# Performance work log

Hardware: AMD Instinct MI355X
Metric: run time of the kernel (lower is better)

## Reference

```python
import jax, jax.numpy as jnp
import numpy as np

B, N, K = 2, 8192, 16
D_IN, D_OUT = 32, 128
EPS = 1e-5


def _bn(x, gamma, beta):
    # x: (B, C, L); BatchNorm1d training-mode stats over (B, L)
    mean = x.mean(axis=(0, 2), keepdims=True)
    var = x.var(axis=(0, 2), keepdims=True)
    return gamma[None, :, None] * (x - mean) * jax.lax.rsqrt(var + EPS) + beta[None, :, None]


def _shared_mlp(x, w, b, gamma, beta, act):
    # SharedMLP: 1x1 Conv1d (channel GEMM) + BN + activation. x: (B, Cin, L)
    y = jnp.einsum('oi,bil->bol', w, x) + b[None, :, None]
    return act(_bn(y, gamma, beta))


def _attentive_pool(x, w, b):
    # x: (B, C, N, K); per-(b,n,k) Linear over C, softmax over K, weighted sum over K
    scores = jnp.einsum('oc,bcnk->bonk', w, x) + b[None, :, None, None]
    scores = jax.nn.softmax(scores, axis=-1)
    return jnp.sum(scores * x, axis=-1)  # (B, C, N)  (torch keeps K=1 dim; squeezed by SharedMLP reshape)


def _knn(coords, k):
    # brute-force squared-L2 KNN excluding self (faiss IndexFlatL2 semantics)
    sq = jnp.sum(coords * coords, axis=-1)  # (B, N)
    d2 = sq[:, :, None] + sq[:, None, :] - 2.0 * jnp.einsum('bid,bjd->bij', coords, coords)
    n = coords.shape[1]
    d2 = jnp.where(jnp.eye(n, dtype=bool)[None], jnp.inf, d2)
    neg, idx = jax.lax.top_k(-d2, k)  # ascending squared distance
    return idx, jnp.maximum(-neg, 0.0)


def _lse(coords, features, idx, dist, w, b, gamma, beta):
    # LocalSpatialEncoding: gather neighbor coords, build 10-ch relative features, MLP, concat
    Bq, Nq, Kq = idx.shape
    neighbor = jax.vmap(lambda c, i: c[i])(coords, idx)  # (B, N, K, 3)
    center = jnp.broadcast_to(coords[:, :, None, :], neighbor.shape)
    rel = center - neighbor
    spatial = jnp.concatenate([center, neighbor, rel, dist[..., None]], axis=-1)  # (B, N, K, 10)
    spatial = spatial.transpose(0, 3, 1, 2).reshape(Bq, 10, Nq * Kq)
    sf = _shared_mlp(spatial, w, b, gamma, beta, jax.nn.relu).reshape(Bq, -1, Nq, Kq)
    feat = jnp.broadcast_to(features[..., None], (Bq, features.shape[1], Nq, Kq))
    return jnp.concatenate([sf, feat], axis=1)


def _forward(coords, features,
             mlp1_w, mlp1_b, mlp1_g, mlp1_bt,
             lse1_w, lse1_b, lse1_g, lse1_bt,
             mlpp1_w, mlpp1_b, mlpp1_g, mlpp1_bt,
             lse2_w, lse2_b, lse2_g, lse2_bt,
             mlp2_w, mlp2_b, mlp2_g, mlp2_bt,
             res_w, res_b, res_g, res_bt,
             pool1_w, pool1_b, pool2_w, pool2_b):
    # faiss output is detached in torch (numpy round-trip) -> stop_gradient
    idx, dist = _knn(jax.lax.stop_gradient(coords), K)
    lrelu02 = lambda v: jnp.where(v >= 0, v, 0.2 * v)   # LeakyReLU(0.2)
    lrelu01 = lambda v: jnp.where(v >= 0, v, 0.01 * v)  # default LeakyReLU
    x = _shared_mlp(features, mlp1_w, mlp1_b, mlp1_g, mlp1_bt, lrelu02)      # (B, 64, N)
    x = _lse(coords, x, idx, dist, lse1_w, lse1_b, lse1_g, lse1_bt)          # (B, 128, N, K)
    x = _attentive_pool(x, pool1_w, pool1_b)                                  # (B, 128, N)
    x = _shared_mlp(x, mlpp1_w, mlpp1_b, mlpp1_g, mlpp1_bt, jax.nn.relu)     # (B, 32, N)
    x = _lse(coords, x, idx, dist, lse2_w, lse2_b, lse2_g, lse2_bt)          # (B, 64, N, K)
    x = _attentive_pool(x, pool2_w, pool2_b)                                  # (B, 64, N)
    x_main = _shared_mlp(x, mlp2_w, mlp2_b, mlp2_g, mlp2_bt, jax.nn.relu)    # (B, 128, N)
    resid = _shared_mlp(features, res_w, res_b, res_g, res_bt, jax.nn.relu)  # (B, 128, N)
    return lrelu01(jnp.concatenate([x_main, resid], axis=1))                 # (B, 256, N)


def setup_inputs() -> dict:
    key = jax.random.key(0)
    ks = iter(jax.random.split(key, 64))

    def lin(ci, co):
        w = jax.random.normal(next(ks), (co, ci), jnp.float32) / np.float32(np.sqrt(ci))
        b = jax.random.normal(next(ks), (co,), jnp.float32) * 0.01
        return w, b

    inp = {}
    inp['coords'] = jax.random.normal(next(ks), (B, N, 3), jnp.float32)
    inp['features'] = jax.random.normal(next(ks), (B, D_IN, N), jnp.float32)
    for name, ci, co in [('mlp1', D_IN, D_OUT // 2), ('lse1', 10, D_OUT // 2),
                         ('mlpp1', D_OUT, D_OUT // 4), ('lse2', 10, D_OUT // 4),
                         ('mlp2', D_OUT // 2, D_OUT), ('res', D_IN, D_OUT)]:
        w, b = lin(ci, co)
        inp[name + '_w'], inp[name + '_b'] = w, b
        inp[name + '_g'] = jnp.ones((co,), jnp.float32)
        inp[name + '_bt'] = jnp.zeros((co,), jnp.float32)
    for name, c in [('pool1', D_OUT), ('pool2', D_OUT // 2)]:
        w, b = lin(c, c)
        inp[name + '_w'], inp[name + '_b'] = w, b
    return inp


def reference(coords, features,
              mlp1_w, mlp1_b, mlp1_g, mlp1_bt,
              lse1_w, lse1_b, lse1_g, lse1_bt,
              mlpp1_w, mlpp1_b, mlpp1_g, mlpp1_bt,
              lse2_w, lse2_b, lse2_g, lse2_bt,
              mlp2_w, mlp2_b, mlp2_g, mlp2_bt,
              res_w, res_b, res_g, res_bt,
              pool1_w, pool1_b, pool2_w, pool2_b):
    return _forward(coords, features,
                    mlp1_w, mlp1_b, mlp1_g, mlp1_bt,
                    lse1_w, lse1_b, lse1_g, lse1_bt,
                    mlpp1_w, mlpp1_b, mlpp1_g, mlpp1_bt,
                    lse2_w, lse2_b, lse2_g, lse2_bt,
                    mlp2_w, mlp2_b, mlp2_g, mlp2_bt,
                    res_w, res_b, res_g, res_bt,
                    pool1_w, pool1_b, pool2_w, pool2_b)
```

## Files before the change

kernel.cpp:

```cpp
#include <hip/hip_runtime.h>

static constexpr int N_ = 8192;
static constexpr int B_ = 2;
static constexpr int K_ = 16;

typedef __attribute__((ext_vector_type(8))) short bf16x8;
typedef __attribute__((ext_vector_type(4))) float f32x4;

__device__ __forceinline__ short f2bf(float f) {
  unsigned int u = __float_as_uint(f);
  unsigned int r = (u + 0x7FFFu + ((u >> 16) & 1u)) >> 16;
  return (short)r;
}
__device__ __forceinline__ float bf2f(short h) {
  return __uint_as_float(((unsigned int)(unsigned short)h) << 16);
}

__global__ __launch_bounds__(512) void knn_kernel(const float* __restrict__ coords,
                                                  const int tbeg, const int tend,
                                                  float* __restrict__ skd, int* __restrict__ ski,
                                                  int* __restrict__ oidx, float* __restrict__ odist) {
  __shared__ float4 pts[2048];
  const int b = blockIdx.y;
  const int wv = threadIdx.x >> 6;
  const int lane = threadIdx.x & 63;
  const int q = blockIdx.x * 8 + wv;
  const float* cb = coords + (size_t)b * N_ * 3;
  const float qx = cb[q * 3 + 0], qy = cb[q * 3 + 1], qz = cb[q * 3 + 2];
  const float qsq = fmaf(qx, qx, fmaf(qy, qy, qz * qz));
  const int qblk = q & ~63;
  const unsigned long long qbit = ~(1ull << (q & 63));
  float kd = INFINITY;
  int ki = 0;
  if (tbeg > 0 && lane < 16) {
    kd = skd[((size_t)b * N_ + q) * K_ + lane];
    ki = ski[((size_t)b * N_ + q) * K_ + lane];
  }
  float tau = __shfl(kd, 15);
  for (int t0 = tbeg; t0 < tend; t0 += 2048) {
    __syncthreads();
    for (int i = threadIdx.x; i < 2048; i += 512) {
      const int p = t0 + i;
      const float x = cb[p * 3 + 0], y = cb[p * 3 + 1], z = cb[p * 3 + 2];
      pts[i] = make_float4(x, y, z, fmaf(x, x, fmaf(y, y, z * z)));
    }
    __syncthreads();
    for (int s = 0; s < 2048; s += 64) {
      const float4 p = pts[s + lane];
      const int base = t0 + s;
      const float dot = fmaf(qx, p.x, fmaf(qy, p.y, qz * p.z));
      const float d2 = fmaf(-2.0f, dot, qsq + p.w);
      unsigned long long m = __ballot(d2 < tau);
      if (base == qblk) m &= qbit;
      while (m) {
// ... 1 lines not shown
        const float dc = __shfl(d2, src);
        const int jc = base + src;
        const float sd = __shfl_up(kd, 1);
        const int si = __shfl_up(ki, 1);
        const bool c1 = kd > dc;
        const bool c2 = (lane > 0) && (sd > dc);
        kd = c1 ? (c2 ? sd : dc) : kd;
        ki = c1 ? (c2 ? si : jc) : ki;
        m &= (m - 1);
        tau = __shfl(kd, 15);
        m &= __ballot(d2 < tau);
      }
    }
  }
  if (lane < 16) {
    if (tend < N_) {
      skd[((size_t)b * N_ + q) * K_ + lane] = kd;
      ski[((size_t)b * N_ + q) * K_ + lane] = ki;
    } else {
      oidx[((size_t)b * N_ + q) * K_ + lane] = ki;
      odist[((size_t)b * N_ + q) * K_ + lane] = fmaxf(kd, 0.0f);
    }
  }
}

__device__ __forceinline__ float snn_get(const float* SNN, int a, int b) {
  const int i = a < b ? a : b, j = a < b ? b : a;
  return SNN[i == 0 ? j : (i == 1 ? 2 + j : 3 + j)];
}
__device__ __forceinline__ float mom_mean(int i, const float* C, const float* SN, float Sd) {
  if (i < 3) return 16.0f * C[i];
  if (i < 6) return SN[i - 3];
  if (i < 9) return 16.0f * C[i - 6] - SN[i - 6];
  return Sd;
}
__device__ __forceinline__ float mom_prod(int i, int j, const float* C, const float* SN,
                                          const float* SNN, float Sd, float Sdd, const float* SND) {
// ... 1 lines not shown
  const int tj = j < 3 ? 0 : (j < 6 ? 1 : (j < 9 ? 2 : 3));
  const int a = (ti == 3) ? 0 : (i - ti * 3);
  const int bb = (tj == 3) ? 0 : (j - tj * 3);
  if (ti == 0 && tj == 0) return 16.0f * C[a] * C[bb];
  if (ti == 0 && tj == 1) return C[a] * SN[bb];
  if (ti == 0 && tj == 2) return C[a] * (16.0f * C[bb] - SN[bb]);
  if (ti == 0 && tj == 3) return C[a] * Sd;
  if (ti == 1 && tj == 1) return snn_get(SNN, a, bb);
  if (ti == 1 && tj == 2) return C[bb] * SN[a] - snn_get(SNN, a, bb);
  if (ti == 1 && tj == 3) return SND[a];
  if (ti == 2 && tj == 2) return 16.0f * C[a] * C[bb] - C[a] * SN[bb] - C[bb] * SN[a] + snn_get(SNN, a, bb);
  if (ti == 2 && tj == 3) return C[a] * Sd - SND[a];
  return Sdd;
}

__global__ __launch_bounds__(256) void moments_kernel(const float* __restrict__ coords,
                                                      const int* __restrict__ knn_i,
                                                      const float* __restrict__ knn_d,
                                                      double* __restrict__ mom) {
  __shared__ float sh[16][65];
  const int k = threadIdx.x & 15;
  const int pl = threadIdx.x >> 4;
  float accv = 0.0f;
  for (int batch = 0; batch < 4; ++batch) {
    const int pt = (blockIdx.x * 4 + batch) * 16 + pl;
    const int b = pt >> 13, n = pt & (N_ - 1);
    const float* cb = coords + (size_t)b * N_ * 3;
    const float cx = cb[n * 3 + 0], cy = cb[n * 3 + 1], cz = cb[n * 3 + 2];
    const int id = knn_i[(size_t)pt * K_ + k];
    const float dd = knn_d[(size_t)pt * K_ + k];
    const float nx = cb[id * 3 + 0], ny = cb[id * 3 + 1], nz = cb[id * 3 + 2];
    float v[14] = {nx, ny, nz, nx * nx, nx * ny, nx * nz, ny * ny, ny * nz, nz * nz,
                   dd, dd * dd, nx * dd, ny * dd, nz * dd};
#pragma unroll
    for (int e = 0; e < 14; ++e) {
      v[e] += __shfl_xor(v[e], 1);
      v[e] += __shfl_xor(v[e], 2);
      v[e] += __shfl_xor(v[e], 4);
      v[e] += __shfl_xor(v[e], 8);
    }
    if (k == 0) {
      const float C[3] = {cx, cy, cz};
      const float SN[3] = {v[0], v[1], v[2]};
      const float SNN[6] = {v[3], v[4], v[5], v[6], v[7], v[8]};
      const float Sd = v[9], Sdd = v[10];
      const float SND[3] = {v[11], v[12], v[13]};
      float m65[65];
      int e = 0;
#pragma unroll
      for (int i = 0; i < 10; ++i) m65[e++] = mom_mean(i, C, SN, Sd);
#pragma unroll
      for (int i = 0; i < 10; ++i)
#pragma unroll
        for (int j = i; j < 10; ++j) m65[e++] = mom_prod(i, j, C, SN, SNN, Sd, Sdd, SND);
#pragma unroll
      for (int q2 = 0; q2 < 65; ++q2) sh[pl][q2] = m65[q2];
    }
    __syncthreads();
    if (threadIdx.x < 65) {
      float s = 0.0f;
#pragma unroll
      for (int r = 0; r < 16; ++r) s += sh[r][threadIdx.x];
      accv += s;
    }
    __syncthreads();
  }
  if (threadIdx.x < 65) atomicAdd(&mom[threadIdx.x], (double)accv);
}

template <int CI, int CO>
__device__ __forceinline__ void conv_frag_seg(const float* __restrict__ w, short* __restrict__ H,
                                              short* __restrict__ L, int tid, int nthr) {
  constexpr int NT = CO / 16;
  for (int i = tid; i < CI * CO; i += nthr) {
    const int j = i & 7, l = (i >> 3) & 63, tmp = i >> 9;
    const int tt = tmp % NT, cc = tmp / NT;
    const int c = cc * 32 + (l >> 4) * 8 + j;
    const int o = tt * 16 + (l & 15);
    const float v = w[o * CI + c];
    const short h = f2bf(v);
    H[i] = h;
    L[i] = f2bf(v - bf2f(h));
  }
}

__global__ __launch_bounds__(256) void convert_kernel(
    const float* __restrict__ pw1, const float* __restrict__ pw2,
    short* __restrict__ wB1, short* __restrict__ wB2,
    const float* __restrict__ wm1, short* __restrict__ f1H, short* __restrict__ f1L,
    const float* __restrict__ wmp, short* __restrict__ f2H, short* __restrict__ f2L,
    const float* __restrict__ wm2, short* __restrict__ f3H, short* __restrict__ f3L,
    const float* __restrict__ wrs, short* __restrict__ fRH, short* __restrict__ fRL) {
  const int blk = blockIdx.x;
  if (blk < 8) {
    const int tid = blk * 256 + threadIdx.x;
    for (int i = tid; i < 128 * 128; i += 2048) wB1[i] = f2bf(pw1[i]);
  } else if (blk < 10) {
    const int tid = (blk - 8) * 256 + threadIdx.x;
    for (int i = tid; i < 64 * 64; i += 512) wB2[i] = f2bf(pw2[i]);
  } else if (blk < 12) {
    conv_frag_seg<32, 64>(wm1, f1H, f1L, (blk - 10) * 256 + threadIdx.x, 512);
  } else if (blk < 16) {
    conv_frag_seg<128, 32>(wmp, f2H, f2L, (blk - 12) * 256 + threadIdx.x, 1024);
  } else if (blk < 24) {
    conv_frag_seg<64, 128>(wm2, f3H, f3L, (blk - 16) * 256 + threadIdx.x, 2048);
  } else {
    conv_frag_seg<32, 128>(wrs, fRH, fRL, (blk - 24) * 256 + threadIdx.x, 1024);
  }
}

__global__ void setup_kernel(const double* __restrict__ mom,
                             const float* __restrict__ w1, const float* __restrict__ b1,
                             const float* __restrict__ g1, const float* __restrict__ t1,
                             const float* __restrict__ w2, const float* __restrict__ b2,
                             const float* __restrict__ g2, const float* __restrict__ t2,
                             float* __restrict__ w1f8, float* __restrict__ w2f8) {
  const int t = threadIdx.x;
  __shared__ double mu[10];
  __shared__ double S[10][10];
  const double cnt = (double)B_ * N_ * K_;
  if (t < 10) mu[t] = mom[t] / cnt;
  if (t < 55) {
    int e = t, i = 0;
    while (e >= 10 - i) { e -= 10 - i; ++i; }
    const int j = i + e;
    const double v = mom[10 + t] / cnt;
    S[i][j] = v;
    S[j][i] = v;
  }
  __syncthreads();
  const float *w, *bias, *gg, *bt;
  float *wf;
  int c;
  if (t < 64) { w = w1; bias = b1; gg = g1; bt = t1; wf = w1f8; c = t; }
  else if (t < 96) { w = w2; bias = b2; gg = g2; bt = t2; wf = w2f8; c = t - 64; }
  else return;
  double wd[10];
#pragma unroll
  for (int d = 0; d < 10; ++d) wd[d] = (double)w[c * 10 + d];
  const double cbv = (double)bias[c];
  double mz = cbv;
  for (int d = 0; d < 10; ++d) mz += wd[d] * mu[d];
  double e2 = cbv * cbv;
  for (int d = 0; d < 10; ++d) e2 += 2.0 * cbv * wd[d] * mu[d];
  for (int d = 0; d < 10; ++d)
    for (int e = 0; e < 10; ++e) e2 += wd[d] * wd[e] * S[d][e];
  const double var = e2 - mz * mz;
  const double a = (double)gg[c] / sqrt(var + 1e-5);
  const double shift = (double)bt[c] - a * mz;
  wf[c * 8 + 0] = (float)(a * (wd[0] + wd[6]));
  wf[c * 8 + 1] = (float)(a * (wd[1] + wd[7]));
  wf[c * 8 + 2] = (float)(a * (wd[2] + wd[8]));
  wf[c * 8 + 3] = (float)(a * (wd[3] - wd[6]));
  wf[c * 8 + 4] = (float)(a * (wd[4] - wd[7]));
  wf[c * 8 + 5] = (float)(a * (wd[5] - wd[8]));
  wf[c * 8 + 6] = (float)(a * wd[9]);
  wf[c * 8 + 7] = (float)(a * cbv + shift);
}

template <int CI, int CO, bool ROWMAJ>
__global__ __launch_bounds__(256) void gemm_mfma_kernel(const float* __restrict__ in,
                                                        const short* __restrict__ fragH,
                                                        const short* __restrict__ fragL,
                                                        const float* __restrict__ bias,
                                                        float* __restrict__ out,
                                                        double* __restrict__ sacc) {
  constexpr int NT = CO / 16;
  constexpr int NC = CI / 32;
  __shared__ float part[4][CO][2];
  const int wv = threadIdx.x >> 6, l = threadIdx.x & 63;
  const int col = l & 15, quad = l >> 4;
  const int p0 = blockIdx.x * 64 + wv * 16;
  const int pt = p0 + col;
  f32x4 d[NT];
#pragma unroll
  for (int t = 0; t < NT; ++t) {
    const float bv = bias[t * 16 + col];
    d[t][0] = bv; d[t][1] = bv; d[t][2] = bv; d[t][3] = bv;
  }
#pragma unroll
  for (int cc = 0; cc < NC; ++cc) {
    float xv[8];
    if (ROWMAJ) {
      const float* ip = in + (size_t)pt * CI + cc * 32 + quad * 8;
      *(float4*)&xv[0] = *(const float4*)ip;
      *(float4*)&xv[4] = *(const float4*)(ip + 4);
    } else {
      const int b = pt >> 13, n = pt & (N_ - 1);
      const float* ip = in + ((size_t)b * CI + cc * 32 + quad * 8) * N_ + n;
#pragma unroll
      for (int j = 0; j < 8; ++j) xv[j] = ip[(size_t)j * N_];
    }
    union { bf16x8 v; short u[8]; } AH, AL;
#pragma unroll
    for (int j = 0; j < 8; ++j) {
      const short h = f2bf(xv[j]);
      AH.u[j] = h;
      AL.u[j] = f2bf(xv[j] - bf2f(h));
    }
#pragma unroll
    for (int t = 0; t < NT; ++t) {
      const size_t fo = ((size_t)(cc * NT + t) * 64 + l) * 8;
      const bf16x8 BH = *(const bf16x8*)(fragH + fo);
      const bf16x8 BL = *(const bf16x8*)(fragL + fo);
      d[t] = __builtin_amdgcn_mfma_f32_16x16x32_bf16(AH.v, BH, d[t], 0, 0, 0);
      d[t] = __builtin_amdgcn_mfma_f32_16x16x32_bf16(AH.v, BL, d[t], 0, 0, 0);
      d[t] = __builtin_amdgcn_mfma_f32_16x16x32_bf16(AL.v, BH, d[t], 0, 0, 0);
    }
  }
#pragma unroll
  for (int t = 0; t < NT; ++t) {
#pragma unroll
    for (int r = 0; r < 4; ++r)
      out[(size_t)(p0 + quad * 4 + r) * CO + t * 16 + col] = d[t][r];
    float s1 = d[t][0] + d[t][1] + d[t][2] + d[t][3];
    float s2 = d[t][0] * d[t][0] + d[t][1] * d[t][1] + d[t][2] * d[t][2] + d[t][3] * d[t][3];
    s1 += __shfl_xor(s1, 16); s1 += __shfl_xor(s1, 32);
    s2 += __shfl_xor(s2, 16); s2 += __shfl_xor(s2, 32);
    if (quad == 0) { part[wv][t * 16 + col][0] = s1; part[wv][t * 16 + col][1] = s2; }
  }
  __syncthreads();
  if (threadIdx.x < CO) {
    const int o = threadIdx.x;
    atomicAdd(&sacc[o], (double)(part[0][o][0] + part[1][o][0] + part[2][o][0] + part[3][o][0]));
    atomicAdd(&sacc[CO + o], (double)(part[0][o][1] + part[1][o][1] + part[2][o][1] + part[3][o][1]));
  }
}

template <int CSF, int CF>
__global__ __launch_bounds__(256) void pool_kernel(
    const float* __restrict__ coords, const int* __restrict__ knn_i, const float* __restrict__ knn_d,
    const float* __restrict__ w8,
    const float* __restrict__ feat, const double* __restrict__ sfe,
    const float* __restrict__ gfe, const float* __restrict__ tfe,
    const float slope,
    const short* __restrict__ wB, const float* __restrict__ pb,
    float* __restrict__ out) {
  constexpr int C = CSF + CF;
  constexpr int CP = C + 4;
  constexpr int NT = C / 16;
  constexpr int NC = C / 32;
  __shared__ float xcat[4][16][CP];
  __shared__ float4 sp4[4][16];
  __shared__ float4 spc[4];
  const int g = threadIdx.x >> 6;
  const int l = threadIdx.x & 63;
  const int quad = l >> 4, col = l & 15;
  const int pid = blockIdx.x * 4 + g;
  const int b = pid >> 13, n = pid & (N_ - 1);
  const float* cb = coords + (size_t)b * N_ * 3;

  if (l < 16) {
    const int id = knn_i[(size_t)pid * K_ + l];
    const float dd = knn_d[(size_t)pid * K_ + l];
    const float nx = cb[id * 3 + 0], ny = cb[id * 3 + 1], nz = cb[id * 3 + 2];
    sp4[g][l] = make_float4(nx, ny, nz, dd);
    if (l == 0) spc[g] = make_float4(cb[n * 3 + 0], cb[n * 3 + 1], cb[n * 3 + 2], 0.0f);
  }
  if (l < CF) {
    const double cnt = (double)(B_ * N_);
    const double mean = sfe[l] / cnt;
    const double var = sfe[CF + l] / cnt - mean * mean;
    const double av = (double)gfe[l] / sqrt(var + 1e-5);
    const float af = (float)av;
    const float bfv = (float)((double)tfe[l] - av * mean);
    float v = feat[(size_t)pid * CF + l];
    v = af * v + bfv;
    v = (v >= 0.0f) ? v : slope * v;
#pragma unroll
    for (int j = 0; j < 16; ++j) xcat[g][j][CSF + l] = v;
  }
  __syncthreads();
  if (l < CSF) {
    const float4 wA = *(const float4*)(w8 + l * 8);
    const float4 wBv = *(const float4*)(w8 + l * 8 + 4);
    const float4 C4 = spc[g];
    const float tterm = wBv.w + wA.x * C4.x + wA.y * C4.y + wA.z * C4.z;
#pragma unroll
    for (int k = 0; k < 16; ++k) {
      const float4 nk = sp4[g][k];
      const float z = tterm + wA.w * nk.x + wBv.x * nk.y + wBv.y * nk.z + wBv.z * nk.w;
      xcat[g][k][l] = fmaxf(z, 0.0f);
    }
  }
  __syncthreads();
  f32x4 d[NT];
#pragma unroll
  for (int t = 0; t < NT; ++t) {
// ... 17 lines not shown
#pragma unroll
  for (int t = 0; t < NT; ++t) {
    float mx = fmaxf(fmaxf(d[t][0], d[t][1]), fmaxf(d[t][2], d[t][3]));
    mx = fmaxf(mx, __shfl_xor(mx, 16));
    mx = fmaxf(mx, __shfl_xor(mx, 32));
    float e0 = __expf(d[t][0] - mx), e1 = __expf(d[t][1] - mx);
    float e2 = __expf(d[t][2] - mx), e3 = __expf(d[t][3] - mx);
    float s = e0 + e1 + e2 + e3;
    s += __shfl_xor(s, 16);
    s += __shfl_xor(s, 32);
    const int o = t * 16 + col;
    float part = e0 * xcat[g][quad * 4 + 0][o] + e1 * xcat[g][quad * 4 + 1][o] +
                 e2 * xcat[g][quad * 4 + 2][o] + e3 * xcat[g][quad * 4 + 3][o];
    part += __shfl_xor(part, 16);
    part += __shfl_xor(part, 32);
    if (quad == 0) out[(size_t)pid * C + o] = part / s;
  }
}

__global__ __launch_bounds__(256) void final_kernel(const float* __restrict__ y3,
                                                    const float* __restrict__ yr,
                                                    const double* __restrict__ s3,
                                                    const float* __restrict__ g3, const float* __restrict__ t3,
                                                    const double* __restrict__ sr,
                                                    const float* __restrict__ gr, const float* __restrict__ tr,
                                                    float* __restrict__ out) {
  __shared__ float tile[256 * 17];
  const int blk = blockIdx.x;
  const int b = blk >> 9;
  const int n0 = (blk & 511) << 4;
  const int c = threadIdx.x;
  const float* src;
  const double* sa;
  const float *gp, *tp;
  int cc;
  if (c < 128) { src = y3; sa = s3; gp = g3; tp = t3; cc = c; }
  else { src = yr; sa = sr; gp = gr; tp = tr; cc = c - 128; }
  const double cnt = (double)(B_ * N_);
  const double mean = sa[cc] / cnt;
  const double var = sa[128 + cc] / cnt - mean * mean;
  const double avd = (double)gp[cc] / sqrt(var + 1e-5);
  const float av = (float)avd;
  const float bv = (float)((double)tp[cc] - avd * mean);
#pragma unroll
  for (int nl = 0; nl < 16; ++nl) {
    const float x = av * src[((size_t)(b * N_ + n0 + nl)) * 128 + cc] + bv;
    tile[c * 17 + nl] = fmaxf(x, 0.0f);
  }
  __syncthreads();
  const int np = c & 15, grp = c >> 4;
#pragma unroll
  for (int j = 0; j < 16; ++j) {
    const int c2 = grp * 16 + j;
    out[((size_t)(b * 256 + c2)) * N_ + n0 + np] = tile[c2 * 17 + np];
  }
}

extern "C" void kernel_launch(void* const* d_in, const int* in_sizes, int n_in,
// ... 23 lines not shown
  const float* mlp2_g = (const float*)d_in[20];
  const float* mlp2_t = (const float*)d_in[21];
  const float* res_w = (const float*)d_in[22];
  const float* res_b = (const float*)d_in[23];
  const float* res_g = (const float*)d_in[24];
  const float* res_t = (const float*)d_in[25];
  const float* pool1_w = (const float*)d_in[26];
  const float* pool1_b = (const float*)d_in[27];
  const float* pool2_w = (const float*)d_in[28];
  const float* pool2_b = (const float*)d_in[29];

  float* wsf = (float*)d_ws;
  int* knn_i = (int*)d_ws;
  float* knn_d = wsf + 262144;
  float* y1 = wsf + 524288;
  float* pooled1 = wsf + 1572864;
  float* y2 = wsf + 3670016;
  float* pooled2 = wsf + 4194304;
  float* y3 = wsf + 5242880;
  float* yr = wsf + 7340032;
  double* dacc = (double*)(wsf + 9437184);
  double* mom = dacc;
  double* sacc_mlp1 = dacc + 65;
  double* sacc_mlpp1 = dacc + 193;
  double* sacc_mlp2 = dacc + 257;
  double* sacc_res = dacc + 513;
  float* fpar = wsf + 9437184 + 1600;
  float* w1f8 = fpar;
  float* w2f8 = w1f8 + 512;
  short* wB1 = (short*)(w2f8 + 256);
  short* wB2 = wB1 + 16384;
  short* f1H = wB2 + 4096;
  short* f1L = f1H + 2048;
  short* f2H = f1L + 2048;
  short* f2L = f2H + 4096;
  short* f3H = f2L + 4096;
  short* f3L = f3H + 8192;
  short* fRH = f3L + 8192;
  short* fRL = fRH + 4096;
  float* skd = wsf + 9468224;
  int* ski = (int*)(skd + 262144);

  hipMemsetAsync(dacc, 0, 769 * sizeof(double), stream);
  knn_kernel<<<dim3(N_ / 8, B_), 512, 0, stream>>>(coords, 0, N_ / 2, skd, ski, knn_i, knn_d);
  knn_kernel<<<dim3(N_ / 8, B_), 512, 0, stream>>>(coords, N_ / 2, N_, skd, ski, knn_i, knn_d);
  convert_kernel<<<28, 256, 0, stream>>>(pool1_w, pool2_w, wB1, wB2,
                                         mlp1_w, f1H, f1L, mlpp1_w, f2H, f2L,
                                         mlp2_w, f3H, f3L, res_w, fRH, fRL);
  moments_kernel<<<256, 256, 0, stream>>>(coords, knn_i, knn_d, mom);
  setup_kernel<<<1, 128, 0, stream>>>(mom, lse1_w, lse1_b, lse1_g, lse1_t,
                                      lse2_w, lse2_b, lse2_g, lse2_t, w1f8, w2f8);
  gemm_mfma_kernel<32, 64, false><<<256, 256, 0, stream>>>(features, f1H, f1L, mlp1_b, y1, sacc_mlp1);
  pool_kernel<64, 64><<<B_ * N_ / 4, 256, 0, stream>>>(
      coords, knn_i, knn_d, w1f8, y1, sacc_mlp1, mlp1_g, mlp1_t, 0.2f, wB1, pool1_b, pooled1);
  gemm_mfma_kernel<128, 32, true><<<256, 256, 0, stream>>>(pooled1, f2H, f2L, mlpp1_b, y2, sacc_mlpp1);
  pool_kernel<32, 32><<<B_ * N_ / 4, 256, 0, stream>>>(
      coords, knn_i, knn_d, w2f8, y2, sacc_mlpp1, mlpp1_g, mlpp1_t, 0.0f, wB2, pool2_b, pooled2);
  gemm_mfma_kernel<64, 128, true><<<256, 256, 0, stream>>>(pooled2, f3H, f3L, mlp2_b, y3, sacc_mlp2);
  gemm_mfma_kernel<32, 128, false><<<256, 256, 0, stream>>>(features, fRH, fRL, res_b, yr, sacc_res);
  final_kernel<<<B_ * 512, 256, 0, stream>>>(y3, yr, sacc_mlp2, mlp2_g, mlp2_t,
                                             sacc_res, res_g, res_t, (float*)d_out);
}
```

Before: 414.9 us.

## Fuse post-pool GEMMs into pool kernels and merge launch stages

Merges the two KNN passes into a single launch over all points, folds the moments computation into the weight-conversion kernel, and runs the mlp1 and residual GEMMs together with the BN setup in one launch. The mlpp1 and mlp2 channel GEMMs move into the pooling kernels, which write y2 and y3 directly and accumulate BN statistics into 64-way partitioned double buffers to reduce atomic contention. This removes several launches and the pooled1/pooled2 round trips through global memory. In exchange the post-pool GEMMs now run as plain FP32 FMAs instead of split-bf16 MFMA, the memset grows, and the final kernel must sum 64 partials per channel.

```diff
diff --git a/kernel.cpp b/kernel.cpp
--- a/kernel.cpp
+++ b/kernel.cpp
@@ -17,9 +17,8 @@
 }
 
 __global__ __launch_bounds__(512) void knn_kernel(const float* __restrict__ coords,
-                                                  const int tbeg, const int tend,
-                                                  float* __restrict__ skd, int* __restrict__ ski,
-                                                  int* __restrict__ oidx, float* __restrict__ odist) {
+                                                  int* __restrict__ oidx,
+                                                  float* __restrict__ odist) {
   __shared__ float4 pts[2048];
   const int b = blockIdx.y;
   const int wv = threadIdx.x >> 6;
@@ -32,12 +31,8 @@
   const unsigned long long qbit = ~(1ull << (q & 63));
   float kd = INFINITY;
   int ki = 0;
-  if (tbeg > 0 && lane < 16) {
-    kd = skd[((size_t)b * N_ + q) * K_ + lane];
-    ki = ski[((size_t)b * N_ + q) * K_ + lane];
-  }
-  float tau = __shfl(kd, 15);
-  for (int t0 = tbeg; t0 < tend; t0 += 2048) {
+  float tau = INFINITY;
+  for (int t0 = 0; t0 < N_; t0 += 2048) {
     __syncthreads();
     for (int i = threadIdx.x; i < 2048; i += 512) {
       const int p = t0 + i;
@@ -69,13 +64,8 @@
     }
   }
   if (lane < 16) {
-    if (tend < N_) {
-      skd[((size_t)b * N_ + q) * K_ + lane] = kd;
-      ski[((size_t)b * N_ + q) * K_ + lane] = ki;
-    } else {
-      oidx[((size_t)b * N_ + q) * K_ + lane] = ki;
-      odist[((size_t)b * N_ + q) * K_ + lane] = fmaxf(kd, 0.0f);
-    }
+    oidx[((size_t)b * N_ + q) * K_ + lane] = ki;
+    odist[((size_t)b * N_ + q) * K_ + lane] = fmaxf(kd, 0.0f);
   }
 }
 
@@ -107,60 +97,6 @@
   return Sdd;
 }
 
-__global__ __launch_bounds__(256) void moments_kernel(const float* __restrict__ coords,
-                                                      const int* __restrict__ knn_i,
-                                                      const float* __restrict__ knn_d,
-                                                      double* __restrict__ mom) {
-  __shared__ float sh[16][65];
-  const int k = threadIdx.x & 15;
-  const int pl = threadIdx.x >> 4;
-  float accv = 0.0f;
-  for (int batch = 0; batch < 4; ++batch) {
-    const int pt = (blockIdx.x * 4 + batch) * 16 + pl;
-    const int b = pt >> 13, n = pt & (N_ - 1);
-    const float* cb = coords + (size_t)b * N_ * 3;
-    const float cx = cb[n * 3 + 0], cy = cb[n * 3 + 1], cz = cb[n * 3 + 2];
-    const int id = knn_i[(size_t)pt * K_ + k];
-    const float dd = knn_d[(size_t)pt * K_ + k];
-    const float nx = cb[id * 3 + 0], ny = cb[id * 3 + 1], nz = cb[id * 3 + 2];
-    float v[14] = {nx, ny, nz, nx * nx, nx * ny, nx * nz, ny * ny, ny * nz, nz * nz,
-                   dd, dd * dd, nx * dd, ny * dd, nz * dd};
-#pragma unroll
-    for (int e = 0; e < 14; ++e) {
-      v[e] += __shfl_xor(v[e], 1);
-      v[e] += __shfl_xor(v[e], 2);
-      v[e] += __shfl_xor(v[e], 4);
-      v[e] += __shfl_xor(v[e], 8);
-    }
-    if (k == 0) {
-      const float C[3] = {cx, cy, cz};
-      const float SN[3] = {v[0], v[1], v[2]};
-      const float SNN[6] = {v[3], v[4], v[5], v[6], v[7], v[8]};
-      const float Sd = v[9], Sdd = v[10];
-      const float SND[3] = {v[11], v[12], v[13]};
-      float m65[65];
-      int e = 0;
-#pragma unroll
-      for (int i = 0; i < 10; ++i) m65[e++] = mom_mean(i, C, SN, Sd);
-#pragma unroll
-      for (int i = 0; i < 10; ++i)
-#pragma unroll
-        for (int j = i; j < 10; ++j) m65[e++] = mom_prod(i, j, C, SN, SNN, Sd, Sdd, SND);
-#pragma unroll
-      for (int q2 = 0; q2 < 65; ++q2) sh[pl][q2] = m65[q2];
-    }
-    __syncthreads();
-    if (threadIdx.x < 65) {
-      float s = 0.0f;
-#pragma unroll
-      for (int r = 0; r < 16; ++r) s += sh[r][threadIdx.x];
-      accv += s;
-    }
-    __syncthreads();
-  }
-  if (threadIdx.x < 65) atomicAdd(&mom[threadIdx.x], (double)accv);
-}
-
 template <int CI, int CO>
 __device__ __forceinline__ void conv_frag_seg(const float* __restrict__ w, short* __restrict__ H,
                                               short* __restrict__ L, int tid, int nthr) {
@@ -177,40 +113,165 @@
   }
 }
 
-__global__ __launch_bounds__(256) void convert_kernel(
+__global__ __launch_bounds__(256) void prep_kernel(
     const float* __restrict__ pw1, const float* __restrict__ pw2,
     short* __restrict__ wB1, short* __restrict__ wB2,
     const float* __restrict__ wm1, short* __restrict__ f1H, short* __restrict__ f1L,
-    const float* __restrict__ wmp, short* __restrict__ f2H, short* __restrict__ f2L,
-    const float* __restrict__ wm2, short* __restrict__ f3H, short* __restrict__ f3L,
-    const float* __restrict__ wrs, short* __restrict__ fRH, short* __restrict__ fRL) {
+    const float* __restrict__ wrs, short* __restrict__ fRH, short* __restrict__ fRL,
+    const float* __restrict__ coords, const int* __restrict__ knn_i,
+    const float* __restrict__ knn_d, double* __restrict__ mom) {
   const int blk = blockIdx.x;
   if (blk < 8) {
-    const int tid = blk * 256 + threadIdx.x;
-    for (int i = tid; i < 128 * 128; i += 2048) wB1[i] = f2bf(pw1[i]);
-  } else if (blk < 10) {
-    const int tid = (blk - 8) * 256 + threadIdx.x;
-    for (int i = tid; i < 64 * 64; i += 512) wB2[i] = f2bf(pw2[i]);
-  } else if (blk < 12) {
-    conv_frag_seg<32, 64>(wm1, f1H, f1L, (blk - 10) * 256 + threadIdx.x, 512);
-  } else if (blk < 16) {
-    conv_frag_seg<128, 32>(wmp, f2H, f2L, (blk - 12) * 256 + threadIdx.x, 1024);
-  } else if (blk < 24) {
-    conv_frag_seg<64, 128>(wm2, f3H, f3L, (blk - 16) * 256 + threadIdx.x, 2048);
-  } else {
-    conv_frag_seg<32, 128>(wrs, fRH, fRL, (blk - 24) * 256 + threadIdx.x, 1024);
-  }
-}
-
-__global__ void setup_kernel(const double* __restrict__ mom,
-                             const float* __restrict__ w1, const float* __restrict__ b1,
-                             const float* __restrict__ g1, const float* __restrict__ t1,
-                             const float* __restrict__ w2, const float* __restrict__ b2,
-                             const float* __restrict__ g2, const float* __restrict__ t2,
-                             float* __restrict__ w1f8, float* __restrict__ w2f8) {
+    if (blk < 4) {
+      for (int i = blk * 256 + threadIdx.x; i < 128 * 128; i += 1024) wB1[i] = f2bf(pw1[i]);
+    } else if (blk == 4) {
+      for (int i = threadIdx.x; i < 64 * 64; i += 256) wB2[i] = f2bf(pw2[i]);
+    } else if (blk == 5) {
+      conv_frag_seg<32, 64>(wm1, f1H, f1L, threadIdx.x, 256);
+    } else {
+      conv_frag_seg<32, 128>(wrs, fRH, fRL, (blk - 6) * 256 + threadIdx.x, 512);
+    }
+    return;
+  }
+  __shared__ float sh[16][65];
+  const int mb = blk - 8;
+  const int k = threadIdx.x & 15;
+  const int pl = threadIdx.x >> 4;
+  float accv = 0.0f;
+  for (int batch = 0; batch < 4; ++batch) {
+    const int pt = (mb * 4 + batch) * 16 + pl;
+    const int b = pt >> 13, n = pt & (N_ - 1);
+    const float* cb = coords + (size_t)b * N_ * 3;
+    const float cx = cb[n * 3 + 0], cy = cb[n * 3 + 1], cz = cb[n * 3 + 2];
+    const int id = knn_i[(size_t)pt * K_ + k];
+    const float dd = knn_d[(size_t)pt * K_ + k];
+    const float nx = cb[id * 3 + 0], ny = cb[id * 3 + 1], nz = cb[id * 3 + 2];
+    float v[14] = {nx, ny, nz, nx * nx, nx * ny, nx * nz, ny * ny, ny * nz, nz * nz,
+                   dd, dd * dd, nx * dd, ny * dd, nz * dd};
+#pragma unroll
+    for (int e = 0; e < 14; ++e) {
+      v[e] += __shfl_xor(v[e], 1);
+      v[e] += __shfl_xor(v[e], 2);
+      v[e] += __shfl_xor(v[e], 4);
+      v[e] += __shfl_xor(v[e], 8);
+    }
+    if (k == 0) {
+      const float C[3] = {cx, cy, cz};
+      const float SN[3] = {v[0], v[1], v[2]};
+      const float SNN[6] = {v[3], v[4], v[5], v[6], v[7], v[8]};
+      const float Sd = v[9], Sdd = v[10];
+      const float SND[3] = {v[11], v[12], v[13]};
+      float m65[65];
+      int e = 0;
+#pragma unroll
+      for (int i = 0; i < 10; ++i) m65[e++] = mom_mean(i, C, SN, Sd);
+#pragma unroll
+      for (int i = 0; i < 10; ++i)
+#pragma unroll
+        for (int j = i; j < 10; ++j) m65[e++] = mom_prod(i, j, C, SN, SNN, Sd, Sdd, SND);
+#pragma unroll
+      for (int q2 = 0; q2 < 65; ++q2) sh[pl][q2] = m65[q2];
+    }
+    __syncthreads();
+    if (threadIdx.x < 65) {
+      float s = 0.0f;
+#pragma unroll
+      for (int r = 0; r < 16; ++r) s += sh[r][threadIdx.x];
+      accv += s;
+    }
+    __syncthreads();
+  }
+  if (threadIdx.x < 65) atomicAdd(&mom[threadIdx.x], (double)accv);
+}
+
+template <int CI, int CO>
+__device__ __forceinline__ void gemm_body(const float* __restrict__ in,
+                                          const short* __restrict__ fragH,
+                                          const short* __restrict__ fragL,
+                                          const float* __restrict__ bias,
+                                          float* __restrict__ out,
+                                          double* __restrict__ sacc,
+                                          int blk, void* smem) {
+  constexpr int NT = CO / 16;
+  constexpr int NC = CI / 32;
+  float (*part)[CO][2] = (float (*)[CO][2])smem;
+  const int wv = threadIdx.x >> 6, l = threadIdx.x & 63;
+  const int col = l & 15, quad = l >> 4;
+  const int p0 = blk * 64 + wv * 16;
+  const int pt = p0 + col;
+  f32x4 d[NT];
+#pragma unroll
+  for (int t = 0; t < NT; ++t) {
+    const float bv = bias[t * 16 + col];
+    d[t][0] = bv; d[t][1] = bv; d[t][2] = bv; d[t][3] = bv;
+  }
+#pragma unroll
+  for (int cc = 0; cc < NC; ++cc) {
+    const int b = pt >> 13, n = pt & (N_ - 1);
+    const float* ip = in + ((size_t)b * CI + cc * 32 + quad * 8) * N_ + n;
+    float xv[8];
+#pragma unroll
+    for (int j = 0; j < 8; ++j) xv[j] = ip[(size_t)j * N_];
+    union { bf16x8 v; short u[8]; } AH, AL;
+#pragma unroll
+    for (int j = 0; j < 8; ++j) {
+      const short h = f2bf(xv[j]);
+      AH.u[j] = h;
+      AL.u[j] = f2bf(xv[j] - bf2f(h));
+    }
+#pragma unroll
+    for (int t = 0; t < NT; ++t) {
+      const size_t fo = ((size_t)(cc * NT + t) * 64 + l) * 8;
+      const bf16x8 BH = *(const bf16x8*)(fragH + fo);
+      const bf16x8 BL = *(const bf16x8*)(fragL + fo);
+      d[t] = __builtin_amdgcn_mfma_f32_16x16x32_bf16(AH.v, BH, d[t], 0, 0, 0);
+      d[t] = __builtin_amdgcn_mfma_f32_16x16x32_bf16(AH.v, BL, d[t], 0, 0, 0);
+      d[t] = __builtin_amdgcn_mfma_f32_16x16x32_bf16(AL.v, BH, d[t], 0, 0, 0);
+    }
+  }
+#pragma unroll
+  for (int t = 0; t < NT; ++t) {
+#pragma unroll
+    for (int r = 0; r < 4; ++r)
+      out[(size_t)(p0 + quad * 4 + r) * CO + t * 16 + col] = d[t][r];
+    float s1 = d[t][0] + d[t][1] + d[t][2] + d[t][3];
+    float s2 = d[t][0] * d[t][0] + d[t][1] * d[t][1] + d[t][2] * d[t][2] + d[t][3] * d[t][3];
+    s1 += __shfl_xor(s1, 16); s1 += __shfl_xor(s1, 32);
+    s2 += __shfl_xor(s2, 16); s2 += __shfl_xor(s2, 32);
+    if (quad == 0) { part[wv][t * 16 + col][0] = s1; part[wv][t * 16 + col][1] = s2; }
+  }
+  __syncthreads();
+  if (threadIdx.x < CO) {
+    const int o = threadIdx.x;
+    atomicAdd(&sacc[o], (double)(part[0][o][0] + part[1][o][0] + part[2][o][0] + part[3][o][0]));
+    atomicAdd(&sacc[CO + o], (double)(part[0][o][1] + part[1][o][1] + part[2][o][1] + part[3][o][1]));
+  }
+}
+
+__global__ __launch_bounds__(256) void gemmA_kernel(
+    const float* __restrict__ features,
+    const short* __restrict__ f1H, const short* __restrict__ f1L,
+    const float* __restrict__ mlp1_b, float* __restrict__ y1, double* __restrict__ sacc1,
+    const short* __restrict__ fRH, const short* __restrict__ fRL,
+    const float* __restrict__ res_b, float* __restrict__ yr, double* __restrict__ saccR,
+    const double* __restrict__ mom,
+    const float* __restrict__ w1, const float* __restrict__ b1,
+    const float* __restrict__ g1, const float* __restrict__ t1,
+    const float* __restrict__ w2, const float* __restrict__ b2,
+    const float* __restrict__ g2, const float* __restrict__ t2,
+    float* __restrict__ w1f8, float* __restrict__ w2f8) {
+  __shared__ char smem[4 * 128 * 2 * 4];
+  if (blockIdx.x < 256) {
+    gemm_body<32, 64>(features, f1H, f1L, mlp1_b, y1, sacc1, blockIdx.x, smem);
+    return;
+  }
+  if (blockIdx.x < 512) {
+    gemm_body<32, 128>(features, fRH, fRL, res_b, yr, saccR, blockIdx.x - 256, smem);
+    return;
+  }
   const int t = threadIdx.x;
-  __shared__ double mu[10];
-  __shared__ double S[10][10];
+  double* mu = (double*)smem;
+  double* S = mu + 10;
   const double cnt = (double)B_ * N_ * K_;
   if (t < 10) mu[t] = mom[t] / cnt;
   if (t < 55) {
@@ -218,8 +279,8 @@
     while (e >= 10 - i) { e -= 10 - i; ++i; }
     const int j = i + e;
     const double v = mom[10 + t] / cnt;
-    S[i][j] = v;
-    S[j][i] = v;
+    S[i * 10 + j] = v;
+    S[j * 10 + i] = v;
   }
   __syncthreads();
   const float *w, *bias, *gg, *bt;
@@ -237,7 +298,7 @@
   double e2 = cbv * cbv;
   for (int d = 0; d < 10; ++d) e2 += 2.0 * cbv * wd[d] * mu[d];
   for (int d = 0; d < 10; ++d)
-    for (int e = 0; e < 10; ++e) e2 += wd[d] * wd[e] * S[d][e];
+    for (int e = 0; e < 10; ++e) e2 += wd[d] * wd[e] * S[d * 10 + e];
   const double var = e2 - mz * mz;
   const double a = (double)gg[c] / sqrt(var + 1e-5);
   const double shift = (double)bt[c] - a * mz;
@@ -251,91 +312,20 @@
   wf[c * 8 + 7] = (float)(a * cbv + shift);
 }
 
-template <int CI, int CO, bool ROWMAJ>
-__global__ __launch_bounds__(256) void gemm_mfma_kernel(const float* __restrict__ in,
-                                                        const short* __restrict__ fragH,
-                                                        const short* __restrict__ fragL,
-                                                        const float* __restrict__ bias,
-                                                        float* __restrict__ out,
-                                                        double* __restrict__ sacc) {
-  constexpr int NT = CO / 16;
-  constexpr int NC = CI / 32;
-  __shared__ float part[4][CO][2];
-  const int wv = threadIdx.x >> 6, l = threadIdx.x & 63;
-  const int col = l & 15, quad = l >> 4;
-  const int p0 = blockIdx.x * 64 + wv * 16;
-  const int pt = p0 + col;
-  f32x4 d[NT];
-#pragma unroll
-  for (int t = 0; t < NT; ++t) {
-    const float bv = bias[t * 16 + col];
-    d[t][0] = bv; d[t][1] = bv; d[t][2] = bv; d[t][3] = bv;
-  }
-#pragma unroll
-  for (int cc = 0; cc < NC; ++cc) {
-    float xv[8];
-    if (ROWMAJ) {
-      const float* ip = in + (size_t)pt * CI + cc * 32 + quad * 8;
-      *(float4*)&xv[0] = *(const float4*)ip;
-      *(float4*)&xv[4] = *(const float4*)(ip + 4);
-    } else {
-      const int b = pt >> 13, n = pt & (N_ - 1);
-      const float* ip = in + ((size_t)b * CI + cc * 32 + quad * 8) * N_ + n;
-#pragma unroll
-      for (int j = 0; j < 8; ++j) xv[j] = ip[(size_t)j * N_];
-    }
-    union { bf16x8 v; short u[8]; } AH, AL;
-#pragma unroll
-    for (int j = 0; j < 8; ++j) {
-      const short h = f2bf(xv[j]);
-      AH.u[j] = h;
-      AL.u[j] = f2bf(xv[j] - bf2f(h));
-    }
-#pragma unroll
-    for (int t = 0; t < NT; ++t) {
-      const size_t fo = ((size_t)(cc * NT + t) * 64 + l) * 8;
-      const bf16x8 BH = *(const bf16x8*)(fragH + fo);
-      const bf16x8 BL = *(const bf16x8*)(fragL + fo);
-      d[t] = __builtin_amdgcn_mfma_f32_16x16x32_bf16(AH.v, BH, d[t], 0, 0, 0);
-      d[t] = __builtin_amdgcn_mfma_f32_16x16x32_bf16(AH.v, BL, d[t], 0, 0, 0);
-      d[t] = __builtin_amdgcn_mfma_f32_16x16x32_bf16(AL.v, BH, d[t], 0, 0, 0);
-    }
-  }
-#pragma unroll
-  for (int t = 0; t < NT; ++t) {
-#pragma unroll
-    for (int r = 0; r < 4; ++r)
-      out[(size_t)(p0 + quad * 4 + r) * CO + t * 16 + col] = d[t][r];
-    float s1 = d[t][0] + d[t][1] + d[t][2] + d[t][3];
-    float s2 = d[t][0] * d[t][0] + d[t][1] * d[t][1] + d[t][2] * d[t][2] + d[t][3] * d[t][3];
-    s1 += __shfl_xor(s1, 16); s1 += __shfl_xor(s1, 32);
-    s2 += __shfl_xor(s2, 16); s2 += __shfl_xor(s2, 32);
-    if (quad == 0) { part[wv][t * 16 + col][0] = s1; part[wv][t * 16 + col][1] = s2; }
-  }
-  __syncthreads();
-  if (threadIdx.x < CO) {
-    const int o = threadIdx.x;
-    atomicAdd(&sacc[o], (double)(part[0][o][0] + part[1][o][0] + part[2][o][0] + part[3][o][0]));
-    atomicAdd(&sacc[CO + o], (double)(part[0][o][1] + part[1][o][1] + part[2][o][1] + part[3][o][1]));
-  }
-}
-
-template <int CSF, int CF>
-__global__ __launch_bounds__(256) void pool_kernel(
+__global__ __launch_bounds__(256) void pool1_kernel(
     const float* __restrict__ coords, const int* __restrict__ knn_i, const float* __restrict__ knn_d,
     const float* __restrict__ w8,
     const float* __restrict__ feat, const double* __restrict__ sfe,
     const float* __restrict__ gfe, const float* __restrict__ tfe,
-    const float slope,
     const short* __restrict__ wB, const float* __restrict__ pb,
-    float* __restrict__ out) {
-  constexpr int C = CSF + CF;
-  constexpr int CP = C + 4;
-  constexpr int NT = C / 16;
-  constexpr int NC = C / 32;
+    const float* __restrict__ w2, const float* __restrict__ b2,
+    float* __restrict__ y2, double* __restrict__ y2part) {
+  constexpr int CSF = 64, CF = 64, C = 128, CP = 132, NT = 8, NC = 4;
   __shared__ float xcat[4][16][CP];
   __shared__ float4 sp4[4][16];
   __shared__ float4 spc[4];
+  __shared__ float plds[4][C];
+  __shared__ float sh2[4][32][2];
   const int g = threadIdx.x >> 6;
   const int l = threadIdx.x & 63;
   const int quad = l >> 4, col = l & 15;
@@ -346,11 +336,10 @@
   if (l < 16) {
     const int id = knn_i[(size_t)pid * K_ + l];
     const float dd = knn_d[(size_t)pid * K_ + l];
-    const float nx = cb[id * 3 + 0], ny = cb[id * 3 + 1], nz = cb[id * 3 + 2];
-    sp4[g][l] = make_float4(nx, ny, nz, dd);
+    sp4[g][l] = make_float4(cb[id * 3 + 0], cb[id * 3 + 1], cb[id * 3 + 2], dd);
     if (l == 0) spc[g] = make_float4(cb[n * 3 + 0], cb[n * 3 + 1], cb[n * 3 + 2], 0.0f);
   }
-  if (l < CF) {
+  {
     const double cnt = (double)(B_ * N_);
     const double mean = sfe[l] / cnt;
     const double var = sfe[CF + l] / cnt - mean * mean;
@@ -359,12 +348,12 @@
     const float bfv = (float)((double)tfe[l] - av * mean);
     float v = feat[(size_t)pid * CF + l];
     v = af * v + bfv;
-    v = (v >= 0.0f) ? v : slope * v;
+    v = (v >= 0.0f) ? v : 0.2f * v;
 #pragma unroll
     for (int j = 0; j < 16; ++j) xcat[g][j][CSF + l] = v;
   }
   __syncthreads();
-  if (l < CSF) {
+  {
     const float4 wA = *(const float4*)(w8 + l * 8);
     const float4 wBv = *(const float4*)(w8 + l * 8 + 4);
     const float4 C4 = spc[g];
@@ -412,13 +401,164 @@
                  e2 * xcat[g][quad * 4 + 2][o] + e3 * xcat[g][quad * 4 + 3][o];
     part += __shfl_xor(part, 16);
     part += __shfl_xor(part, 32);
-    if (quad == 0) out[(size_t)pid * C + o] = part / s;
+    if (quad == 0) plds[g][o] = part / s;
+  }
+  __syncthreads();
+  if (l < 32) {
+    float acc = b2[l];
+    const float* wr = w2 + l * 128;
+#pragma unroll 8
+    for (int c4 = 0; c4 < 32; ++c4) {
+      const float4 w4 = *(const float4*)(wr + c4 * 4);
+      const float4 p4 = *(const float4*)&plds[g][c4 * 4];
+      acc += w4.x * p4.x + w4.y * p4.y + w4.z * p4.z + w4.w * p4.w;
+    }
+    y2[(size_t)pid * 32 + l] = acc;
+    sh2[g][l][0] = acc;
+    sh2[g][l][1] = acc * acc;
+  }
+  __syncthreads();
+  if (threadIdx.x < 32) {
+    const int o = threadIdx.x;
+    const double s1 = (double)sh2[0][o][0] + sh2[1][o][0] + sh2[2][o][0] + sh2[3][o][0];
+    const double s2 = (double)sh2[0][o][1] + sh2[1][o][1] + sh2[2][o][1] + sh2[3][o][1];
+    const int gid = blockIdx.x & 63;
+    atomicAdd(&y2part[(size_t)(gid * 32 + o) * 2 + 0], s1);
+    atomicAdd(&y2part[(size_t)(gid * 32 + o) * 2 + 1], s2);
+  }
+}
+
+__global__ __launch_bounds__(256) void pool2_kernel(
+    const float* __restrict__ coords, const int* __restrict__ knn_i, const float* __restrict__ knn_d,
+    const float* __restrict__ w8,
+    const float* __restrict__ feat, const double* __restrict__ y2part,
+    const float* __restrict__ gfe, const float* __restrict__ tfe,
+    const short* __restrict__ wB, const float* __restrict__ pb,
+    const float* __restrict__ w3, const float* __restrict__ b3,
+    float* __restrict__ y3, double* __restrict__ y3part) {
+  constexpr int CSF = 32, CF = 32, C = 64, CP = 68, NT = 4, NC = 2;
+  __shared__ float xcat[4][16][CP];
+  __shared__ float4 sp4[4][16];
+  __shared__ float4 spc[4];
+  __shared__ float afs[32], bfs[32];
+  __shared__ float p2lds[4][C];
+  __shared__ float sh3[4][128][2];
+  const int g = threadIdx.x >> 6;
+  const int l = threadIdx.x & 63;
+  const int quad = l >> 4, col = l & 15;
+  const int pid = blockIdx.x * 4 + g;
+  const int b = pid >> 13, n = pid & (N_ - 1);
+  const float* cb = coords + (size_t)b * N_ * 3;
+
+  if (l < 16) {
+    const int id = knn_i[(size_t)pid * K_ + l];
+    const float dd = knn_d[(size_t)pid * K_ + l];
+    sp4[g][l] = make_float4(cb[id * 3 + 0], cb[id * 3 + 1], cb[id * 3 + 2], dd);
+    if (l == 0) spc[g] = make_float4(cb[n * 3 + 0], cb[n * 3 + 1], cb[n * 3 + 2], 0.0f);
+  }
+  if (threadIdx.x < 32) {
+    double s1 = 0.0, s2 = 0.0;
+    for (int gg = 0; gg < 64; ++gg) {
+      s1 += y2part[(size_t)(gg * 32 + threadIdx.x) * 2 + 0];
+      s2 += y2part[(size_t)(gg * 32 + threadIdx.x) * 2 + 1];
+    }
+    const double cnt = (double)(B_ * N_);
+    const double mean = s1 / cnt;
+    const double var = s2 / cnt - mean * mean;
+    const double av = (double)gfe[threadIdx.x] / sqrt(var + 1e-5);
+    afs[threadIdx.x] = (float)av;
+    bfs[threadIdx.x] = (float)((double)tfe[threadIdx.x] - av * mean);
+  }
+  __syncthreads();
+  if (l < CF) {
+    float v = feat[(size_t)pid * CF + l];
+    v = afs[l] * v + bfs[l];
+    v = fmaxf(v, 0.0f);
+#pragma unroll
+    for (int j = 0; j < 16; ++j) xcat[g][j][CSF + l] = v;
+  }
+  if (l < CSF) {
+    const float4 wA = *(const float4*)(w8 + l * 8);
+    const float4 wBv = *(const float4*)(w8 + l * 8 + 4);
+    const float4 C4 = spc[g];
+    const float tterm = wBv.w + wA.x * C4.x + wA.y * C4.y + wA.z * C4.z;
+#pragma unroll
+    for (int k = 0; k < 16; ++k) {
+      const float4 nk = sp4[g][k];
+      const float z = tterm + wA.w * nk.x + wBv.x * nk.y + wBv.y * nk.z + wBv.z * nk.w;
+      xcat[g][k][l] = fmaxf(z, 0.0f);
+    }
+  }
+  __syncthreads();
+  f32x4 d[NT];
+#pragma unroll
+  for (int t = 0; t < NT; ++t) {
+    const float pbv = pb[t * 16 + col];
+    d[t][0] = pbv; d[t][1] = pbv; d[t][2] = pbv; d[t][3] = pbv;
+  }
+#pragma unroll
+  for (int cc = 0; cc < NC; ++cc) {
+    const float* xr = &xcat[g][col][cc * 32 + quad * 8];
+    const float4 xa = *(const float4*)xr;
+    const float4 xb = *(const float4*)(xr + 4);
+    union { bf16x8 v; short u[8]; } A;
+    A.u[0] = f2bf(xa.x); A.u[1] = f2bf(xa.y); A.u[2] = f2bf(xa.z); A.u[3] = f2bf(xa.w);
+    A.u[4] = f2bf(xb.x); A.u[5] = f2bf(xb.y); A.u[6] = f2bf(xb.z); A.u[7] = f2bf(xb.w);
+#pragma unroll
+    for (int t = 0; t < NT; ++t) {
+      const bf16x8 Bv = *(const bf16x8*)(wB + (size_t)(t * 16 + col) * C + cc * 32 + quad * 8);
+      d[t] = __builtin_amdgcn_mfma_f32_16x16x32_bf16(A.v, Bv, d[t], 0, 0, 0);
+    }
+  }
+#pragma unroll
+  for (int t = 0; t < NT; ++t) {
+    float mx = fmaxf(fmaxf(d[t][0], d[t][1]), fmaxf(d[t][2], d[t][3]));
+    mx = fmaxf(mx, __shfl_xor(mx, 16));
+    mx = fmaxf(mx, __shfl_xor(mx, 32));
+    float e0 = __expf(d[t][0] - mx), e1 = __expf(d[t][1] - mx);
+    float e2 = __expf(d[t][2] - mx), e3 = __expf(d[t][3] - mx);
+    float s = e0 + e1 + e2 + e3;
+    s += __shfl_xor(s, 16);
+    s += __shfl_xor(s, 32);
+    const int o = t * 16 + col;
+    float part = e0 * xcat[g][quad * 4 + 0][o] + e1 * xcat[g][quad * 4 + 1][o] +
+                 e2 * xcat[g][quad * 4 + 2][o] + e3 * xcat[g][quad * 4 + 3][o];
+    part += __shfl_xor(part, 16);
+    part += __shfl_xor(part, 32);
+    if (quad == 0) p2lds[g][o] = part / s;
+  }
+  __syncthreads();
+  {
+    const int o0 = 2 * l, o1 = 2 * l + 1;
+    float a0 = b3[o0], a1 = b3[o1];
+    const float* w0 = w3 + (size_t)o0 * 64;
+    const float* w1 = w3 + (size_t)o1 * 64;
+#pragma unroll 4
+    for (int c4 = 0; c4 < 16; ++c4) {
+      const float4 p4 = *(const float4*)&p2lds[g][c4 * 4];
+      const float4 wa = *(const float4*)(w0 + c4 * 4);
+      const float4 wb = *(const float4*)(w1 + c4 * 4);
+      a0 += wa.x * p4.x + wa.y * p4.y + wa.z * p4.z + wa.w * p4.w;
+      a1 += wb.x * p4.x + wb.y * p4.y + wb.z * p4.z + wb.w * p4.w;
+    }
+    *(float2*)(y3 + (size_t)pid * 128 + o0) = make_float2(a0, a1);
+    sh3[g][o0][0] = a0; sh3[g][o0][1] = a0 * a0;
+    sh3[g][o1][0] = a1; sh3[g][o1][1] = a1 * a1;
+  }
+  __syncthreads();
+  if (threadIdx.x < 128) {
+    const int o = threadIdx.x;
+    const double s1 = (double)sh3[0][o][0] + sh3[1][o][0] + sh3[2][o][0] + sh3[3][o][0];
+    const double s2 = (double)sh3[0][o][1] + sh3[1][o][1] + sh3[2][o][1] + sh3[3][o][1];
+    const int gid = blockIdx.x & 63;
+    atomicAdd(&y3part[(size_t)(gid * 128 + o) * 2 + 0], s1);
+    atomicAdd(&y3part[(size_t)(gid * 128 + o) * 2 + 1], s2);
   }
 }
 
 __global__ __launch_bounds__(256) void final_kernel(const float* __restrict__ y3,
                                                     const float* __restrict__ yr,
-                                                    const double* __restrict__ s3,
+                                                    const double* __restrict__ y3part,
                                                     const float* __restrict__ g3, const float* __restrict__ t3,
                                                     const double* __restrict__ sr,
                                                     const float* __restrict__ gr, const float* __restrict__ tr,
@@ -429,17 +569,29 @@
   const int n0 = (blk & 511) << 4;
   const int c = threadIdx.x;
   const float* src;
-  const double* sa;
-  const float *gp, *tp;
+  float av, bv;
   int cc;
-  if (c < 128) { src = y3; sa = s3; gp = g3; tp = t3; cc = c; }
-  else { src = yr; sa = sr; gp = gr; tp = tr; cc = c - 128; }
   const double cnt = (double)(B_ * N_);
-  const double mean = sa[cc] / cnt;
-  const double var = sa[128 + cc] / cnt - mean * mean;
-  const double avd = (double)gp[cc] / sqrt(var + 1e-5);
-  const float av = (float)avd;
-  const float bv = (float)((double)tp[cc] - avd * mean);
+  if (c < 128) {
+    src = y3; cc = c;
+    double s1 = 0.0, s2 = 0.0;
+    for (int gg = 0; gg < 64; ++gg) {
+      s1 += y3part[(size_t)(gg * 128 + cc) * 2 + 0];
+      s2 += y3part[(size_t)(gg * 128 + cc) * 2 + 1];
+    }
+    const double mean = s1 / cnt;
+    const double var = s2 / cnt - mean * mean;
+    const double avd = (double)g3[cc] / sqrt(var + 1e-5);
+    av = (float)avd;
+    bv = (float)((double)t3[cc] - avd * mean);
+  } else {
+    src = yr; cc = c - 128;
+    const double mean = sr[cc] / cnt;
+    const double var = sr[128 + cc] / cnt - mean * mean;
+    const double avd = (double)gr[cc] / sqrt(var + 1e-5);
+    av = (float)avd;
+    bv = (float)((double)tr[cc] - avd * mean);
+  }
 #pragma unroll
   for (int nl = 0; nl < 16; ++nl) {
     const float x = av * src[((size_t)(b * N_ + n0 + nl)) * 128 + cc] + bv;
@@ -493,50 +645,40 @@
   int* knn_i = (int*)d_ws;
   float* knn_d = wsf + 262144;
   float* y1 = wsf + 524288;
-  float* pooled1 = wsf + 1572864;
-  float* y2 = wsf + 3670016;
-  float* pooled2 = wsf + 4194304;
-  float* y3 = wsf + 5242880;
-  float* yr = wsf + 7340032;
-  double* dacc = (double*)(wsf + 9437184);
+  float* y2 = wsf + 1572864;
+  float* y3 = wsf + 2097152;
+  float* yr = wsf + 4194304;
+  double* dacc = (double*)(wsf + 6291456);
   double* mom = dacc;
   double* sacc_mlp1 = dacc + 65;
-  double* sacc_mlpp1 = dacc + 193;
-  double* sacc_mlp2 = dacc + 257;
-  double* sacc_res = dacc + 513;
-  float* fpar = wsf + 9437184 + 1600;
+  double* sacc_res = dacc + 193;
+  double* y2part = dacc + 449;
+  double* y3part = dacc + 4545;
+  float* fpar = wsf + 6333440;
   float* w1f8 = fpar;
   float* w2f8 = w1f8 + 512;
   short* wB1 = (short*)(w2f8 + 256);
   short* wB2 = wB1 + 16384;
   short* f1H = wB2 + 4096;
   short* f1L = f1H + 2048;
-  short* f2H = f1L + 2048;
-  short* f2L = f2H + 4096;
-  short* f3H = f2L + 4096;
-  short* f3L = f3H + 8192;
-  short* fRH = f3L + 8192;
+  short* fRH = f1L + 2048;
   short* fRL = fRH + 4096;
-  float* skd = wsf + 9468224;
-  int* ski = (int*)(skd + 262144);
-
-  hipMemsetAsync(dacc, 0, 769 * sizeof(double), stream);
-  knn_kernel<<<dim3(N_ / 8, B_), 512, 0, stream>>>(coords, 0, N_ / 2, skd, ski, knn_i, knn_d);
-  knn_kernel<<<dim3(N_ / 8, B_), 512, 0, stream>>>(coords, N_ / 2, N_, skd, ski, knn_i, knn_d);
-  convert_kernel<<<28, 256, 0, stream>>>(pool1_w, pool2_w, wB1, wB2,
-                                         mlp1_w, f1H, f1L, mlpp1_w, f2H, f2L,
-                                         mlp2_w, f3H, f3L, res_w, fRH, fRL);
-  moments_kernel<<<256, 256, 0, stream>>>(coords, knn_i, knn_d, mom);
-  setup_kernel<<<1, 128, 0, stream>>>(mom, lse1_w, lse1_b, lse1_g, lse1_t,
-                                      lse2_w, lse2_b, lse2_g, lse2_t, w1f8, w2f8);
-  gemm_mfma_kernel<32, 64, false><<<256, 256, 0, stream>>>(features, f1H, f1L, mlp1_b, y1, sacc_mlp1);
-  pool_kernel<64, 64><<<B_ * N_ / 4, 256, 0, stream>>>(
-      coords, knn_i, knn_d, w1f8, y1, sacc_mlp1, mlp1_g, mlp1_t, 0.2f, wB1, pool1_b, pooled1);
-  gemm_mfma_kernel<128, 32, true><<<256, 256, 0, stream>>>(pooled1, f2H, f2L, mlpp1_b, y2, sacc_mlpp1);
-  pool_kernel<32, 32><<<B_ * N_ / 4, 256, 0, stream>>>(
-      coords, knn_i, knn_d, w2f8, y2, sacc_mlpp1, mlpp1_g, mlpp1_t, 0.0f, wB2, pool2_b, pooled2);
-  gemm_mfma_kernel<64, 128, true><<<256, 256, 0, stream>>>(pooled2, f3H, f3L, mlp2_b, y3, sacc_mlp2);
-  gemm_mfma_kernel<32, 128, false><<<256, 256, 0, stream>>>(features, fRH, fRL, res_b, yr, sacc_res);
-  final_kernel<<<B_ * 512, 256, 0, stream>>>(y3, yr, sacc_mlp2, mlp2_g, mlp2_t,
+
+  hipMemsetAsync(dacc, 0, 20929 * sizeof(double), stream);
+  knn_kernel<<<dim3(N_ / 8, B_), 512, 0, stream>>>(coords, knn_i, knn_d);
+  prep_kernel<<<8 + 256, 256, 0, stream>>>(pool1_w, pool2_w, wB1, wB2,
+                                           mlp1_w, f1H, f1L, res_w, fRH, fRL,
+                                           coords, knn_i, knn_d, mom);
+  gemmA_kernel<<<513, 256, 0, stream>>>(features, f1H, f1L, mlp1_b, y1, sacc_mlp1,
+                                        fRH, fRL, res_b, yr, sacc_res, mom,
+                                        lse1_w, lse1_b, lse1_g, lse1_t,
+                                        lse2_w, lse2_b, lse2_g, lse2_t, w1f8, w2f8);
+  pool1_kernel<<<B_ * N_ / 4, 256, 0, stream>>>(coords, knn_i, knn_d, w1f8,
+                                                y1, sacc_mlp1, mlp1_g, mlp1_t,
+                                                wB1, pool1_b, mlpp1_w, mlpp1_b, y2, y2part);
+  pool2_kernel<<<B_ * N_ / 4, 256, 0, stream>>>(coords, knn_i, knn_d, w2f8,
+                                                y2, y2part, mlpp1_g, mlpp1_t,
+                                                wB2, pool2_b, mlp2_w, mlp2_b, y3, y3part);
+  final_kernel<<<B_ * 512, 256, 0, stream>>>(y3, yr, y3part, mlp2_g, mlp2_t,
                                              sacc_res, res_g, res_t, (float*)d_out);
 }
```

Result: slower. 479.8 us (+15.6%).
